# Optimization experiments

Hardware: AMD Instinct MI355X
Metric: run time of the kernel (lower is better)

## Reference

```python
import jax, jax.numpy as jnp
import numpy as np

E = 512
H = 8
D = E // H  # head_dims = 64
MAXREL = 512


def setup_inputs() -> dict:
    key = jax.random.key(0)
    ks = jax.random.split(key, 12)
    B, L = 4, 1024
    s_lin = float(np.sqrt(6.0 / (D + D)))  # xavier uniform for (D,D)
    s_fc = float(np.sqrt(6.0 / (E + E)))
    s_tab = float(np.sqrt(6.0 / (2 * MAXREL + 1 + D)))
    return {
        "query": jax.random.normal(ks[0], (B, L, E), jnp.float32),
        "key": jax.random.normal(ks[1], (B, L, E), jnp.float32),
        "value": jax.random.normal(ks[2], (B, L, E), jnp.float32),
        "mask": jax.random.randint(ks[3], (B, 1, 1, L), 0, 2, jnp.int32),
        "Wq": jax.random.uniform(ks[4], (D, D), jnp.float32, -s_lin, s_lin),
        "bq": jnp.zeros((D,), jnp.float32),
        "Wk": jax.random.uniform(ks[5], (D, D), jnp.float32, -s_lin, s_lin),
        "bk": jnp.zeros((D,), jnp.float32),
        "Wv": jax.random.uniform(ks[6], (D, D), jnp.float32, -s_lin, s_lin),
        "bv": jnp.zeros((D,), jnp.float32),
        "Wfc": jax.random.uniform(ks[7], (E, E), jnp.float32, -s_fc, s_fc),
        "bfc": jnp.zeros((E,), jnp.float32),
        "rel_k_table": jax.random.uniform(ks[8], (2 * MAXREL + 1, D), jnp.float32, -s_tab, s_tab),
        "rel_v_table": jax.random.uniform(ks[9], (2 * MAXREL + 1, D), jnp.float32, -s_tab, s_tab),
    }


def _rel_indices(length_q, length_k):
    dist = jnp.arange(length_k)[None, :] - jnp.arange(length_q)[:, None]
    return jnp.clip(dist, -MAXREL, MAXREL) + MAXREL  # [Q, K]


def reference(query, key, value, mask, Wq, bq, Wk, bk, Wv, bv, Wfc, bfc, rel_k_table, rel_v_table):
    B, Q, _ = query.shape
    K = key.shape[1]
    q = query.reshape(B, Q, H, D) @ Wq.T + bq  # per-head linear (same weights all heads)
    k = key.reshape(B, K, H, D) @ Wk.T + bk
    v = value.reshape(B, K, H, D) @ Wv.T + bv

    scores = jnp.einsum("bqhd,bkhd->bhqk", q, k)  # [B,H,Q,K]
    scores = jnp.where(mask == 0, jnp.float32(-1e20), scores)  # mask BEFORE bias & scale, as in source

    idx = _rel_indices(Q, K)
    a_key = rel_k_table[idx]    # [Q,K,D]
    a_val = rel_v_table[idx]    # [Q,K,D]
    scores = scores + jnp.einsum("bqhd,qkd->bhqk", q, a_key)

    attn = jax.nn.softmax(scores / jnp.sqrt(jnp.float32(D)), axis=-1)

    out = jnp.einsum("bhqk,bkhd->bqhd", attn, v)  # standard AV
    out = out + jnp.einsum("bhqk,qkd->bqhd", attn, a_val)  # relative-position value term
    out = out.reshape(B, Q, H * D)
    return out @ Wfc.T + bfc
```

## Files before the change

### kernel.cpp

```cpp
#include <hip/hip_runtime.h>
#include <math.h>

#define BB 4
#define LL 1024
#define EE 512
#define HH 8
#define DD 64
#define MAXREL 512

typedef unsigned short u16;
typedef __attribute__((ext_vector_type(8))) short bf16x8;
typedef __attribute__((ext_vector_type(4))) float f32x4;

__device__ __forceinline__ u16 f2bf(float f) {
    unsigned int u = __float_as_uint(f);
    unsigned int r = (u + 0x7FFFu + ((u >> 16) & 1u)) >> 16;
    return (u16)r;
}
__device__ __forceinline__ float bf2f(u16 b) {
    return __uint_as_float(((unsigned int)b) << 16);
}
__device__ __forceinline__ bf16x8 ldf8_bf(const float* p) {
    const float4 a = *(const float4*)(p);
    const float4 b = *(const float4*)(p + 4);
    bf16x8 r;
    r[0] = (short)f2bf(a.x); r[1] = (short)f2bf(a.y);
    r[2] = (short)f2bf(a.z); r[3] = (short)f2bf(a.w);
    r[4] = (short)f2bf(b.x); r[5] = (short)f2bf(b.y);
    r[6] = (short)f2bf(b.z); r[7] = (short)f2bf(b.w);
    return r;
}

#define MF(A, B, C) __builtin_amdgcn_mfma_f32_16x16x32_bf16((A), (B), (C), 0, 0, 0)

__global__ __launch_bounds__(256) void proj_mfma_kernel(
    const float* __restrict__ q_in, const float* __restrict__ k_in, const float* __restrict__ v_in,
    const float* __restrict__ Wq, const float* __restrict__ bq,
    const float* __restrict__ Wk, const float* __restrict__ bk,
    const float* __restrict__ Wv, const float* __restrict__ bv,
    u16* __restrict__ qb, u16* __restrict__ kb, u16* __restrict__ vtb)
{
    int bh = blockIdx.x; int b = bh >> 3; int h = bh & 7;
    int l0 = blockIdx.y * 64;
    int t = threadIdx.x; int w = t >> 6; int lane = t & 63;
    int lg = lane >> 4, lc = lane & 15;
    int lt = l0 + w * 16;

    bf16x8 wq[4][2], wk[4][2], wv[4][2];
    #pragma unroll
    for (int dt = 0; dt < 4; ++dt)
        #pragma unroll
        for (int kc = 0; kc < 2; ++kc) {
            int d = dt * 16 + lc, ko = kc * 32 + lg * 8;
            wq[dt][kc] = ldf8_bf(Wq + d * DD + ko);
            wk[dt][kc] = ldf8_bf(Wk + d * DD + ko);
            wv[dt][kc] = ldf8_bf(Wv + d * DD + ko);
        }
    size_t xrow = ((size_t)b * LL + lt + lc) * EE + h * DD;
    bf16x8 xq[2], xk[2], xv[2];
    #pragma unroll
    for (int kc = 0; kc < 2; ++kc) {
        int ko = kc * 32 + lg * 8;
        xq[kc] = ldf8_bf(q_in + xrow + ko);
        xk[kc] = ldf8_bf(k_in + xrow + ko);
        xv[kc] = ldf8_bf(v_in + xrow + ko);
    }

    f32x4 aq[4] = {}, ak[4] = {}, av[4] = {};
    #pragma unroll
    for (int dt = 0; dt < 4; ++dt) {
        aq[dt] = MF(wq[dt][0], xq[0], aq[dt]);
        aq[dt] = MF(wq[dt][1], xq[1], aq[dt]);
        ak[dt] = MF(wk[dt][0], xk[0], ak[dt]);
        ak[dt] = MF(wk[dt][1], xk[1], ak[dt]);
        av[dt] = MF(xv[0], wv[dt][0], av[dt]);
        av[dt] = MF(xv[1], wv[dt][1], av[dt]);
    }

    #pragma unroll
    for (int dt = 0; dt < 4; ++dt) {
        u16 tq[4], tk[4], tv[4];
        #pragma unroll
        for (int r = 0; r < 4; ++r) {
            int d = dt * 16 + lg * 4 + r;
            tq[r] = f2bf(aq[dt][r] + bq[d]);
            tk[r] = f2bf(ak[dt][r] + bk[d]);
            tv[r] = f2bf(av[dt][r] + bv[dt * 16 + lc]);
        }
        size_t o = ((size_t)bh * LL + lt + lc) * DD + dt * 16 + lg * 4;
        *(uint2*)&qb[o] = *(uint2*)tq;
        *(uint2*)&kb[o] = *(uint2*)tk;
        size_t ov = ((size_t)bh * DD + dt * 16 + lc) * LL + lt + lg * 4;
        *(uint2*)&vtb[ov] = *(uint2*)tv;
    }
}

__global__ __launch_bounds__(256) void prep_kernel(
    const float* __restrict__ relk, const float* __restrict__ relv, const float* __restrict__ Wfc,
    u16* __restrict__ relk_pad, u16* __restrict__ relvt_pad, u16* __restrict__ wfcb)
{
    int idx = blockIdx.x * 256 + threadIdx.x;
    if (idx < 2048 * DD) {
        int r = idx >> 6, d = idx & 63;
        int j = r - 512; j = j < 0 ? 0 : (j > 2 * MAXREL ? 2 * MAXREL : j);
        relk_pad[idx] = f2bf(relk[j * DD + d]);
        int dd = idx >> 11, c = idx & 2047;
        int j2 = c - 512; j2 = j2 < 0 ? 0 : (j2 > 2 * MAXREL ? 2 * MAXREL : j2);
        relvt_pad[idx] = f2bf(relv[j2 * DD + dd]);
    }
    if (idx < EE * EE) wfcb[idx] = f2bf(Wfc[idx]);
}

__global__ __launch_bounds__(256) void attn_mfma_kernel(
    const u16* __restrict__ qb, const u16* __restrict__ kb, const u16* __restrict__ vtb,
    const int* __restrict__ mask,
    const u16* __restrict__ relk_pad, const u16* __restrict__ relvt_pad,
    u16* __restrict__ attn_out)
{
    __shared__ __align__(16) char smem[48384];
    u16* Ks   = (u16*)(smem);
    u16* Vts  = (u16*)(smem + 9216);
    u16* RVts = (u16*)(smem + 18432);
    float* lred = (float*)(smem + 48128);
    float* obuf = (float*)smem;

    int bh = blockIdx.x, b = bh >> 3, h = bh & 7;
    int q0 = blockIdx.y * 32;
    int t = threadIdx.x, lane = t & 63, w = t >> 6;
    int rw = w & 1, cw = w >> 1;
    int rbase = rw * 16, c0a = cw * 32;
    int lg = lane >> 4, lc = lane & 15;
    int ub = c0a - rbase + 16;
    size_t bhL = (size_t)bh * LL;
    const u16* kb_bh = kb + bhL * DD;
    const u16* vt_bh = vtb + (size_t)bh * DD * LL;
    const int* mk_b = mask + b * LL;
    u16* Pw  = (u16*)(smem + 33792) + w * 640;
    u16* Pqw = (u16*)(smem + 38912) + w * 1152;

    int su0 = t, su1 = t + 256;
    int sr0 = su0 >> 3, ss0 = (su0 & 7) * 8;
    int sr1 = su1 >> 3, ss1 = (su1 & 7) * 8;
    int rv_row = t >> 2, rv_q = (t & 3) * 24;
    const u16* rvg = relvt_pad + (size_t)rv_row * 2048 + rv_q;
    u16* rvl = RVts + rv_row * 120 + rv_q;
    const u16* rk_base = relk_pad + (size_t)(ub + lc) * DD + lg * 8;

    const u16* qrow = qb + (bhL + q0 + rbase + lc) * DD;
    bf16x8 qf0 = *(const bf16x8*)&qrow[lg * 8];
    bf16x8 qf1 = *(const bf16x8*)&qrow[32 + lg * 8];

    #pragma unroll
    for (int i = 0; i < 3; ++i) {
        int u = lane + i * 64;
        if (u < 144) *(uint4*)&Pqw[u * 8] = make_uint4(0, 0, 0, 0);
    }
    if (t < 192) {
        int row = t / 3, j = t - row * 3;
        *(uint4*)&RVts[row * 120 + 96 + j * 8] = make_uint4(0, 0, 0, 0);
    }
    int sb0 = 992 - q0;
    *(uint4*)&Ks[sr0 * 72 + ss0]  = *(const uint4*)&kb_bh[(size_t)sr0 * DD + ss0];
    *(uint4*)&Ks[sr1 * 72 + ss1]  = *(const uint4*)&kb_bh[(size_t)sr1 * DD + ss1];
    *(uint4*)&Vts[sr0 * 72 + ss0] = *(const uint4*)&vt_bh[(size_t)sr0 * LL + ss0];
    *(uint4*)&Vts[sr1 * 72 + ss1] = *(const uint4*)&vt_bh[(size_t)sr1 * LL + ss1];
    *(uint4*)&rvl[0]  = *(const uint4*)&rvg[sb0];
    *(uint4*)&rvl[8]  = *(const uint4*)&rvg[sb0 + 8];
    *(uint4*)&rvl[16] = *(const uint4*)&rvg[sb0 + 16];
    bf16x8 rk0, rk1, rk2, rk3, rk4, rk5;
    {
        const u16* rkp = rk_base + (size_t)sb0 * DD;
        rk0 = *(const bf16x8*)&rkp[0];
        rk1 = *(const bf16x8*)&rkp[32];
        rk2 = *(const bf16x8*)&rkp[16 * DD];
        rk3 = *(const bf16x8*)&rkp[16 * DD + 32];
        rk4 = *(const bf16x8*)&rkp[32 * DD];
        rk5 = *(const bf16x8*)&rkp[32 * DD + 32];
    }
    __syncthreads();

    f32x4 oacc[4] = {};
    float lacc[4] = {0.f, 0.f, 0.f, 0.f};
    int delta0 = lc - lg * 4;

    #pragma unroll 1
    for (int c = 0; c < 16; ++c) {
        int k0 = c * 64;
        int sb = k0 - q0 + 992;
        int mv0 = mk_b[k0 + c0a + lc];
        int mv1 = mk_b[k0 + c0a + 16 + lc];
        uint4 rK0, rK1, rV0, rV1;
        if (c < 15) {
            int k0n = k0 + 64;
            rK0 = *(const uint4*)&kb_bh[(size_t)(k0n + sr0) * DD + ss0];
            rK1 = *(const uint4*)&kb_bh[(size_t)(k0n + sr1) * DD + ss1];
            rV0 = *(const uint4*)&vt_bh[(size_t)sr0 * LL + k0n + ss0];
            rV1 = *(const uint4*)&vt_bh[(size_t)sr1 * LL + k0n + ss1];
        }

        __builtin_amdgcn_s_setprio(1);
        f32x4 s0 = {}, s1 = {};
        {
            const u16* kp0 = &Ks[(c0a + lc) * 72];
            const u16* kp1 = &Ks[(c0a + 16 + lc) * 72];
            s0 = MF(qf0, *(const bf16x8*)&kp0[lg * 8], s0);
            s0 = MF(qf1, *(const bf16x8*)&kp0[32 + lg * 8], s0);
            s1 = MF(qf0, *(const bf16x8*)&kp1[lg * 8], s1);
            s1 = MF(qf1, *(const bf16x8*)&kp1[32 + lg * 8], s1);
        }
        f32x4 g0 = {}, g1 = {}, g2 = {};
        g0 = MF(qf0, rk0, g0); g0 = MF(qf1, rk1, g0);
        g1 = MF(qf0, rk2, g1); g1 = MF(qf1, rk3, g1);
        g2 = MF(qf0, rk4, g2); g2 = MF(qf1, rk5, g2);
        __builtin_amdgcn_s_setprio(0);

        if (c < 15) {
            const u16* rkp = rk_base + (size_t)(sb + 64) * DD;
            rk0 = *(const bf16x8*)&rkp[0];
            rk1 = *(const bf16x8*)&rkp[32];
            rk2 = *(const bf16x8*)&rkp[16 * DD];
            rk3 = *(const bf16x8*)&rkp[16 * DD + 32];
            rk4 = *(const bf16x8*)&rkp[32 * DD];
            rk5 = *(const bf16x8*)&rkp[32 * DD + 32];
        }

        float mb0 = mv0 ? 0.f : -1e20f;
        float mb1 = mv1 ? 0.f : -1e20f;
        #pragma unroll
        for (int r = 0; r < 4; ++r) {
            int d = delta0 - r;
            int src = (lane & 48) | (d & 15);
            float a0 = __shfl(g0[r], src, 64);
            float a1 = __shfl(g1[r], src, 64);
            float a2 = __shfl(g2[r], src, 64);
            float gv0 = (d >= 0) ? a1 : a0;
            float gv1 = (d >= 0) ? a2 : a1;
            float p0 = __expf((s0[r] + mb0 + gv0) * 0.125f);
            float p1 = __expf((s1[r] + mb1 + gv1) * 0.125f);
            u16 pb0 = f2bf(p0), pb1 = f2bf(p1);
            lacc[r] += bf2f(pb0) + bf2f(pb1);
            int row = lg * 4 + r;
            Pw[row * 40 + lc] = pb0;
            Pw[row * 40 + 16 + lc] = pb1;
            Pqw[row * 72 + lc - row + 16] = pb0;
            Pqw[row * 72 + 32 + lc - row] = pb1;
        }
        asm volatile("s_waitcnt lgkmcnt(0)" ::: "memory");
        __builtin_amdgcn_sched_barrier(0);

        bf16x8 pa  = *(const bf16x8*)&Pw[lc * 40 + lg * 8];
        bf16x8 pq0 = *(const bf16x8*)&Pqw[lc * 72 + lg * 8];
        bf16x8 pq1 = *(const bf16x8*)&Pqw[lc * 72 + 32 + lg * 8];

        __builtin_amdgcn_s_setprio(1);
        #pragma unroll
        for (int dt = 0; dt < 4; ++dt) {
            const u16* vp = &Vts[(dt * 16 + lc) * 72 + c0a];
            const u16* rp = &RVts[(dt * 16 + lc) * 120 + ub];
            oacc[dt] = MF(pa,  *(const bf16x8*)&vp[lg * 8], oacc[dt]);
            oacc[dt] = MF(pq0, *(const bf16x8*)&rp[lg * 8], oacc[dt]);
            oacc[dt] = MF(pq1, *(const bf16x8*)&rp[32 + lg * 8], oacc[dt]);
        }
        __builtin_amdgcn_s_setprio(0);

        if (c < 15) {
            int sbn = sb + 64;
            uint4 b0 = *(const uint4*)&rvg[sbn];
            uint4 b1 = *(const uint4*)&rvg[sbn + 8];
            uint4 b2 = *(const uint4*)&rvg[sbn + 16];
            __syncthreads();
            *(uint4*)&Ks[sr0 * 72 + ss0]  = rK0;
            *(uint4*)&Ks[sr1 * 72 + ss1]  = rK1;
            *(uint4*)&Vts[sr0 * 72 + ss0] = rV0;
            *(uint4*)&Vts[sr1 * 72 + ss1] = rV1;
            *(uint4*)&rvl[0]  = b0;
            *(uint4*)&rvl[8]  = b1;
            *(uint4*)&rvl[16] = b2;
            __syncthreads();
        }
    }

    #pragma unroll
    for (int m2 = 1; m2 <= 8; m2 <<= 1) {
        #pragma unroll
        for (int r = 0; r < 4; ++r) lacc[r] += __shfl_xor(lacc[r], m2);
    }
    if (lc == 0) {
        #pragma unroll
        for (int r = 0; r < 4; ++r) lred[cw * 32 + rbase + lg * 4 + r] = lacc[r];
    }
    __syncthreads();
    if (cw == 1) {
        #pragma unroll
        for (int dt = 0; dt < 4; ++dt)
            #pragma unroll
            for (int r = 0; r < 4; ++r)
                obuf[(rbase + lg * 4 + r) * 68 + dt * 16 + lc] = oacc[dt][r];
    }
    __syncthreads();
    if (cw == 0) {
        float inv[4];
        #pragma unroll
        for (int r = 0; r < 4; ++r) {
            int row = rbase + lg * 4 + r;
            inv[r] = 1.0f / (lred[row] + lred[32 + row]);
        }
        #pragma unroll
        for (int dt = 0; dt < 4; ++dt) {
            #pragma unroll
            for (int r = 0; r < 4; ++r) {
                int row = rbase + lg * 4 + r;
                float v = (oacc[dt][r] + obuf[row * 68 + dt * 16 + lc]) * inv[r];
                attn_out[((size_t)b * LL + q0 + row) * EE + h * DD + dt * 16 + lc] = f2bf(v);
            }
        }
    }
}

__global__ __launch_bounds__(256) void fc_mfma_kernel(
    const u16* __restrict__ Xb, const u16* __restrict__ Wb,
    const float* __restrict__ bfc, float* __restrict__ out)
{
    __shared__ u16 As[128][72];
    __shared__ u16 Bs[128][72];
    int m0 = blockIdx.x * 128, n0 = blockIdx.y * 128;
    int t = threadIdx.x, lane = t & 63, w = t >> 6;
    int rw = w & 1, cw = w >> 1;
    int lg = lane >> 4, lc = lane & 15;
    f32x4 acc[4][4] = {};

    for (int kt = 0; kt < EE; kt += 64) {
        __syncthreads();
        #pragma unroll
        for (int i = 0; i < 4; ++i) {
            int unit = i * 256 + t;
            int row = unit >> 3, s = unit & 7;
            *(uint4*)&As[row][s * 8] = *(const uint4*)&Xb[(size_t)(m0 + row) * EE + kt + s * 8];
            *(uint4*)&Bs[row][s * 8] = *(const uint4*)&Wb[(size_t)(n0 + row) * EE + kt + s * 8];
        }
        __syncthreads();
        #pragma unroll
        for (int kc = 0; kc < 2; ++kc) {
            bf16x8 af[4], bf[4];
            #pragma unroll
            for (int i = 0; i < 4; ++i) {
                af[i] = *(const bf16x8*)&As[rw * 64 + i * 16 + lc][kc * 32 + lg * 8];
                bf[i] = *(const bf16x8*)&Bs[cw * 64 + i * 16 + lc][kc * 32 + lg * 8];
            }
            #pragma unroll
            for (int mi = 0; mi < 4; ++mi)
                #pragma unroll
                for (int ni = 0; ni < 4; ++ni)
                    acc[mi][ni] = MF(af[mi], bf[ni], acc[mi][ni]);
        }
    }
    #pragma unroll
    for (int mi = 0; mi < 4; ++mi) {
        #pragma unroll
        for (int ni = 0; ni < 4; ++ni) {
            int n = n0 + cw * 64 + ni * 16 + lc;
            float bias = bfc[n];
            #pragma unroll
            for (int r = 0; r < 4; ++r) {
                int m = m0 + rw * 64 + mi * 16 + lg * 4 + r;
                out[(size_t)m * EE + n] = acc[mi][ni][r] + bias;
            }
        }
    }
}

extern "C" void kernel_launch(void* const* d_in, const int* in_sizes, int n_in,
                              void* d_out, int out_size, void* d_ws, size_t ws_size,
                              hipStream_t stream) {
    const float* query = (const float*)d_in[0];
    const float* key   = (const float*)d_in[1];
    const float* value = (const float*)d_in[2];
    const int*   mask  = (const int*)d_in[3];
    const float* Wq  = (const float*)d_in[4];
    const float* bq  = (const float*)d_in[5];
    const float* Wk  = (const float*)d_in[6];
    const float* bk  = (const float*)d_in[7];
    const float* Wv  = (const float*)d_in[8];
    const float* bv  = (const float*)d_in[9];
    const float* Wfc = (const float*)d_in[10];
    const float* bfc = (const float*)d_in[11];
    const float* relk = (const float*)d_in[12];
    const float* relv = (const float*)d_in[13];
    float* out = (float*)d_out;

    char* ws = (char*)d_ws;
    u16* qb        = (u16*)(ws);
    u16* kb        = (u16*)(ws + (4u << 20));
    u16* vtb       = (u16*)(ws + (8u << 20));
    u16* attnb     = (u16*)(ws + (12u << 20));
    u16* relk_pad  = (u16*)(ws + (16u << 20));
    u16* relvt_pad = (u16*)(ws + (16u << 20) + 262144);
    u16* wfcb      = (u16*)(ws + (16u << 20) + 524288);

    proj_mfma_kernel<<<dim3(BB * HH, LL / 64), 256, 0, stream>>>(
        query, key, value, Wq, bq, Wk, bk, Wv, bv, qb, kb, vtb);
    prep_kernel<<<1024, 256, 0, stream>>>(relk, relv, Wfc, relk_pad, relvt_pad, wfcb);
    attn_mfma_kernel<<<dim3(BB * HH, LL / 32), 256, 0, stream>>>(
        qb, kb, vtb, mask, relk_pad, relvt_pad, attnb);
    fc_mfma_kernel<<<dim3(BB * LL / 128, EE / 128), 256, 0, stream>>>(attnb, wfcb, bfc, out);
}
```

Baseline: 117.1 us.

## Load K fragments directly to registers, prefetch mask, use exp2 with folded scale

```diff
diff --git a/kernel.cpp b/kernel.cpp
--- a/kernel.cpp
+++ b/kernel.cpp
@@ -32,6 +32,7 @@
 }
 
 #define MF(A, B, C) __builtin_amdgcn_mfma_f32_16x16x32_bf16((A), (B), (C), 0, 0, 0)
+#define EXPSC 0.1803368801111244f
 
 __global__ __launch_bounds__(256) void proj_mfma_kernel(
     const float* __restrict__ q_in, const float* __restrict__ k_in, const float* __restrict__ v_in,
@@ -117,11 +118,10 @@
     const u16* __restrict__ relk_pad, const u16* __restrict__ relvt_pad,
     u16* __restrict__ attn_out)
 {
-    __shared__ __align__(16) char smem[48384];
-    u16* Ks   = (u16*)(smem);
-    u16* Vts  = (u16*)(smem + 9216);
-    u16* RVts = (u16*)(smem + 18432);
-    float* lred = (float*)(smem + 48128);
+    __shared__ __align__(16) char smem[39168];
+    u16* Vts  = (u16*)(smem);
+    u16* RVts = (u16*)(smem + 9216);
+    float* lred = (float*)(smem + 38912);
     float* obuf = (float*)smem;
 
     int bh = blockIdx.x, b = bh >> 3, h = bh & 7;
@@ -135,16 +135,16 @@
     const u16* kb_bh = kb + bhL * DD;
     const u16* vt_bh = vtb + (size_t)bh * DD * LL;
     const int* mk_b = mask + b * LL;
-    u16* Pw  = (u16*)(smem + 33792) + w * 640;
-    u16* Pqw = (u16*)(smem + 38912) + w * 1152;
-
-    int su0 = t, su1 = t + 256;
-    int sr0 = su0 >> 3, ss0 = (su0 & 7) * 8;
-    int sr1 = su1 >> 3, ss1 = (su1 & 7) * 8;
+    u16* Pw  = (u16*)(smem + 24576) + w * 640;
+    u16* Pqw = (u16*)(smem + 29696) + w * 1152;
+
+    int sr0 = t >> 3, ss0 = (t & 7) * 8;
+    int sr1 = sr0 + 32;
     int rv_row = t >> 2, rv_q = (t & 3) * 24;
     const u16* rvg = relvt_pad + (size_t)rv_row * 2048 + rv_q;
     u16* rvl = RVts + rv_row * 120 + rv_q;
     const u16* rk_base = relk_pad + (size_t)(ub + lc) * DD + lg * 8;
+    const u16* kf_base = kb_bh + (size_t)(c0a + lc) * DD + lg * 8;
 
     const u16* qrow = qb + (bhL + q0 + rbase + lc) * DD;
     bf16x8 qf0 = *(const bf16x8*)&qrow[lg * 8];
@@ -160,13 +160,15 @@
         *(uint4*)&RVts[row * 120 + 96 + j * 8] = make_uint4(0, 0, 0, 0);
     }
     int sb0 = 992 - q0;
-    *(uint4*)&Ks[sr0 * 72 + ss0]  = *(const uint4*)&kb_bh[(size_t)sr0 * DD + ss0];
-    *(uint4*)&Ks[sr1 * 72 + ss1]  = *(const uint4*)&kb_bh[(size_t)sr1 * DD + ss1];
     *(uint4*)&Vts[sr0 * 72 + ss0] = *(const uint4*)&vt_bh[(size_t)sr0 * LL + ss0];
-    *(uint4*)&Vts[sr1 * 72 + ss1] = *(const uint4*)&vt_bh[(size_t)sr1 * LL + ss1];
+    *(uint4*)&Vts[sr1 * 72 + ss0] = *(const uint4*)&vt_bh[(size_t)sr1 * LL + ss0];
     *(uint4*)&rvl[0]  = *(const uint4*)&rvg[sb0];
     *(uint4*)&rvl[8]  = *(const uint4*)&rvg[sb0 + 8];
     *(uint4*)&rvl[16] = *(const uint4*)&rvg[sb0 + 16];
+    bf16x8 kf0 = *(const bf16x8*)(kf_base);
+    bf16x8 kf1 = *(const bf16x8*)(kf_base + 32);
+    bf16x8 kf2 = *(const bf16x8*)(kf_base + 16 * DD);
+    bf16x8 kf3 = *(const bf16x8*)(kf_base + 16 * DD + 32);
     bf16x8 rk0, rk1, rk2, rk3, rk4, rk5;
     {
         const u16* rkp = rk_base + (size_t)sb0 * DD;
@@ -177,6 +179,8 @@
         rk4 = *(const bf16x8*)&rkp[32 * DD];
         rk5 = *(const bf16x8*)&rkp[32 * DD + 32];
     }
+    float mb0 = (mk_b[c0a + lc] != 0) ? 0.f : -1e20f;
+    float mb1 = (mk_b[c0a + 16 + lc] != 0) ? 0.f : -1e20f;
     __syncthreads();
 
     f32x4 oacc[4] = {};
@@ -187,27 +191,20 @@
     for (int c = 0; c < 16; ++c) {
         int k0 = c * 64;
         int sb = k0 - q0 + 992;
-        int mv0 = mk_b[k0 + c0a + lc];
-        int mv1 = mk_b[k0 + c0a + 16 + lc];
-        uint4 rK0, rK1, rV0, rV1;
+        uint4 rV0, rV1;
+        float mbn0 = 0.f, mbn1 = 0.f;
         if (c < 15) {
             int k0n = k0 + 64;
-            rK0 = *(const uint4*)&kb_bh[(size_t)(k0n + sr0) * DD + ss0];
-            rK1 = *(const uint4*)&kb_bh[(size_t)(k0n + sr1) * DD + ss1];
             rV0 = *(const uint4*)&vt_bh[(size_t)sr0 * LL + k0n + ss0];
-            rV1 = *(const uint4*)&vt_bh[(size_t)sr1 * LL + k0n + ss1];
+            rV1 = *(const uint4*)&vt_bh[(size_t)sr1 * LL + k0n + ss0];
+            mbn0 = (mk_b[k0n + c0a + lc] != 0) ? 0.f : -1e20f;
+            mbn1 = (mk_b[k0n + c0a + 16 + lc] != 0) ? 0.f : -1e20f;
         }
 
         __builtin_amdgcn_s_setprio(1);
         f32x4 s0 = {}, s1 = {};
-        {
-            const u16* kp0 = &Ks[(c0a + lc) * 72];
-            const u16* kp1 = &Ks[(c0a + 16 + lc) * 72];
-            s0 = MF(qf0, *(const bf16x8*)&kp0[lg * 8], s0);
-            s0 = MF(qf1, *(const bf16x8*)&kp0[32 + lg * 8], s0);
-            s1 = MF(qf0, *(const bf16x8*)&kp1[lg * 8], s1);
-            s1 = MF(qf1, *(const bf16x8*)&kp1[32 + lg * 8], s1);
-        }
+        s0 = MF(qf0, kf0, s0); s0 = MF(qf1, kf1, s0);
+        s1 = MF(qf0, kf2, s1); s1 = MF(qf1, kf3, s1);
         f32x4 g0 = {}, g1 = {}, g2 = {};
         g0 = MF(qf0, rk0, g0); g0 = MF(qf1, rk1, g0);
         g1 = MF(qf0, rk2, g1); g1 = MF(qf1, rk3, g1);
@@ -215,6 +212,11 @@
         __builtin_amdgcn_s_setprio(0);
 
         if (c < 15) {
+            const u16* kfp = kf_base + (size_t)(k0 + 64) * DD;
+            kf0 = *(const bf16x8*)(kfp);
+            kf1 = *(const bf16x8*)(kfp + 32);
+            kf2 = *(const bf16x8*)(kfp + 16 * DD);
+            kf3 = *(const bf16x8*)(kfp + 16 * DD + 32);
             const u16* rkp = rk_base + (size_t)(sb + 64) * DD;
             rk0 = *(const bf16x8*)&rkp[0];
             rk1 = *(const bf16x8*)&rkp[32];
@@ -224,8 +226,6 @@
             rk5 = *(const bf16x8*)&rkp[32 * DD + 32];
         }
 
-        float mb0 = mv0 ? 0.f : -1e20f;
-        float mb1 = mv1 ? 0.f : -1e20f;
         #pragma unroll
         for (int r = 0; r < 4; ++r) {
             int d = delta0 - r;
@@ -235,8 +235,8 @@
             float a2 = __shfl(g2[r], src, 64);
             float gv0 = (d >= 0) ? a1 : a0;
             float gv1 = (d >= 0) ? a2 : a1;
-            float p0 = __expf((s0[r] + mb0 + gv0) * 0.125f);
-            float p1 = __expf((s1[r] + mb1 + gv1) * 0.125f);
+            float p0 = exp2f((s0[r] + mb0 + gv0) * EXPSC);
+            float p1 = exp2f((s1[r] + mb1 + gv1) * EXPSC);
             u16 pb0 = f2bf(p0), pb1 = f2bf(p1);
             lacc[r] += bf2f(pb0) + bf2f(pb1);
             int row = lg * 4 + r;
@@ -245,6 +245,7 @@
             Pqw[row * 72 + lc - row + 16] = pb0;
             Pqw[row * 72 + 32 + lc - row] = pb1;
         }
+        mb0 = mbn0; mb1 = mbn1;
         asm volatile("s_waitcnt lgkmcnt(0)" ::: "memory");
         __builtin_amdgcn_sched_barrier(0);
 
@@ -269,10 +270,8 @@
             uint4 b1 = *(const uint4*)&rvg[sbn + 8];
             uint4 b2 = *(const uint4*)&rvg[sbn + 16];
             __syncthreads();
-            *(uint4*)&Ks[sr0 * 72 + ss0]  = rK0;
-            *(uint4*)&Ks[sr1 * 72 + ss1]  = rK1;
             *(uint4*)&Vts[sr0 * 72 + ss0] = rV0;
-            *(uint4*)&Vts[sr1 * 72 + ss1] = rV1;
+            *(uint4*)&Vts[sr1 * 72 + ss0] = rV1;
             *(uint4*)&rvl[0]  = b0;
             *(uint4*)&rvl[8]  = b1;
             *(uint4*)&rvl[16] = b2;
```

New measurement: 135.8 us. +16.0%, slower.

## Double-buffer relative-key fragments and prefetch mask and rel-V tiles a chunk ahead

Applied to the files above, without the earlier changes.

```diff
diff --git a/kernel.cpp b/kernel.cpp
--- a/kernel.cpp
+++ b/kernel.cpp
@@ -32,6 +32,7 @@
 }
 
 #define MF(A, B, C) __builtin_amdgcn_mfma_f32_16x16x32_bf16((A), (B), (C), 0, 0, 0)
+#define EXPSC 0.1803368801111244f
 
 __global__ __launch_bounds__(256) void proj_mfma_kernel(
     const float* __restrict__ q_in, const float* __restrict__ k_in, const float* __restrict__ v_in,
@@ -138,9 +139,8 @@
     u16* Pw  = (u16*)(smem + 33792) + w * 640;
     u16* Pqw = (u16*)(smem + 38912) + w * 1152;
 
-    int su0 = t, su1 = t + 256;
-    int sr0 = su0 >> 3, ss0 = (su0 & 7) * 8;
-    int sr1 = su1 >> 3, ss1 = (su1 & 7) * 8;
+    int sr0 = t >> 3, ss0 = (t & 7) * 8;
+    int sr1 = sr0 + 32;
     int rv_row = t >> 2, rv_q = (t & 3) * 24;
     const u16* rvg = relvt_pad + (size_t)rv_row * 2048 + rv_q;
     u16* rvl = RVts + rv_row * 120 + rv_q;
@@ -161,124 +161,133 @@
     }
     int sb0 = 992 - q0;
     *(uint4*)&Ks[sr0 * 72 + ss0]  = *(const uint4*)&kb_bh[(size_t)sr0 * DD + ss0];
-    *(uint4*)&Ks[sr1 * 72 + ss1]  = *(const uint4*)&kb_bh[(size_t)sr1 * DD + ss1];
+    *(uint4*)&Ks[sr1 * 72 + ss0]  = *(const uint4*)&kb_bh[(size_t)sr1 * DD + ss0];
     *(uint4*)&Vts[sr0 * 72 + ss0] = *(const uint4*)&vt_bh[(size_t)sr0 * LL + ss0];
-    *(uint4*)&Vts[sr1 * 72 + ss1] = *(const uint4*)&vt_bh[(size_t)sr1 * LL + ss1];
+    *(uint4*)&Vts[sr1 * 72 + ss0] = *(const uint4*)&vt_bh[(size_t)sr1 * LL + ss0];
     *(uint4*)&rvl[0]  = *(const uint4*)&rvg[sb0];
     *(uint4*)&rvl[8]  = *(const uint4*)&rvg[sb0 + 8];
     *(uint4*)&rvl[16] = *(const uint4*)&rvg[sb0 + 16];
-    bf16x8 rk0, rk1, rk2, rk3, rk4, rk5;
+    bf16x8 rkA0, rkA1, rkA2, rkA3, rkA4, rkA5;
+    bf16x8 rkB0, rkB1, rkB2, rkB3, rkB4, rkB5;
     {
         const u16* rkp = rk_base + (size_t)sb0 * DD;
-        rk0 = *(const bf16x8*)&rkp[0];
-        rk1 = *(const bf16x8*)&rkp[32];
-        rk2 = *(const bf16x8*)&rkp[16 * DD];
-        rk3 = *(const bf16x8*)&rkp[16 * DD + 32];
-        rk4 = *(const bf16x8*)&rkp[32 * DD];
-        rk5 = *(const bf16x8*)&rkp[32 * DD + 32];
-    }
+        rkA0 = *(const bf16x8*)&rkp[0];
+        rkA1 = *(const bf16x8*)&rkp[32];
+        rkA2 = *(const bf16x8*)&rkp[16 * DD];
+        rkA3 = *(const bf16x8*)&rkp[16 * DD + 32];
+        rkA4 = *(const bf16x8*)&rkp[32 * DD];
+        rkA5 = *(const bf16x8*)&rkp[32 * DD + 32];
+        const u16* rkq = rk_base + (size_t)(sb0 + 64) * DD;
+        rkB0 = *(const bf16x8*)&rkq[0];
+        rkB1 = *(const bf16x8*)&rkq[32];
+        rkB2 = *(const bf16x8*)&rkq[16 * DD];
+        rkB3 = *(const bf16x8*)&rkq[16 * DD + 32];
+        rkB4 = *(const bf16x8*)&rkq[32 * DD];
+        rkB5 = *(const bf16x8*)&rkq[32 * DD + 32];
+    }
+    float mb0 = (mk_b[c0a + lc] != 0) ? 0.f : -1e20f;
+    float mb1 = (mk_b[c0a + 16 + lc] != 0) ? 0.f : -1e20f;
     __syncthreads();
 
     f32x4 oacc[4] = {};
     float lacc[4] = {0.f, 0.f, 0.f, 0.f};
     int delta0 = lc - lg * 4;
 
+#define CHUNK(C, RK0, RK1, RK2, RK3, RK4, RK5) do { \
+    int k0 = (C) * 64; \
+    int sb_ = k0 - q0 + 992; \
+    uint4 rK0, rK1, rV0, rV1, bb0, bb1, bb2; \
+    float mbn0 = 0.f, mbn1 = 0.f; \
+    if ((C) < 15) { \
+        int k0n = k0 + 64; int sbn_ = sb_ + 64; \
+        rK0 = *(const uint4*)&kb_bh[(size_t)(k0n + sr0) * DD + ss0]; \
+        rK1 = *(const uint4*)&kb_bh[(size_t)(k0n + sr1) * DD + ss0]; \
+        rV0 = *(const uint4*)&vt_bh[(size_t)sr0 * LL + k0n + ss0]; \
+        rV1 = *(const uint4*)&vt_bh[(size_t)sr1 * LL + k0n + ss0]; \
+        bb0 = *(const uint4*)&rvg[sbn_]; \
+        bb1 = *(const uint4*)&rvg[sbn_ + 8]; \
+        bb2 = *(const uint4*)&rvg[sbn_ + 16]; \
+        mbn0 = (mk_b[k0n + c0a + lc] != 0) ? 0.f : -1e20f; \
+        mbn1 = (mk_b[k0n + c0a + 16 + lc] != 0) ? 0.f : -1e20f; \
+    } \
+    __builtin_amdgcn_s_setprio(1); \
+    f32x4 s0 = {}, s1 = {}; \
+    { \
+        const u16* kp0 = &Ks[(c0a + lc) * 72]; \
+        const u16* kp1 = &Ks[(c0a + 16 + lc) * 72]; \
+        s0 = MF(qf0, *(const bf16x8*)&kp0[lg * 8], s0); \
+        s0 = MF(qf1, *(const bf16x8*)&kp0[32 + lg * 8], s0); \
+        s1 = MF(qf0, *(const bf16x8*)&kp1[lg * 8], s1); \
+        s1 = MF(qf1, *(const bf16x8*)&kp1[32 + lg * 8], s1); \
+    } \
+    f32x4 g0 = {}, g1 = {}, g2 = {}; \
+    g0 = MF(qf0, RK0, g0); g0 = MF(qf1, RK1, g0); \
+    g1 = MF(qf0, RK2, g1); g1 = MF(qf1, RK3, g1); \
+    g2 = MF(qf0, RK4, g2); g2 = MF(qf1, RK5, g2); \
+    __builtin_amdgcn_s_setprio(0); \
+    if ((C) < 14) { \
+        const u16* rkp_ = rk_base + (size_t)(sb_ + 128) * DD; \
+        RK0 = *(const bf16x8*)&rkp_[0]; \
+        RK1 = *(const bf16x8*)&rkp_[32]; \
+        RK2 = *(const bf16x8*)&rkp_[16 * DD]; \
+        RK3 = *(const bf16x8*)&rkp_[16 * DD + 32]; \
+        RK4 = *(const bf16x8*)&rkp_[32 * DD]; \
+        RK5 = *(const bf16x8*)&rkp_[32 * DD + 32]; \
+    } \
+    _Pragma("unroll") \
+    for (int r = 0; r < 4; ++r) { \
+        int d_ = delta0 - r; \
+        int src = (lane & 48) | (d_ & 15); \
+        float a0 = __shfl(g0[r], src, 64); \
+        float a1 = __shfl(g1[r], src, 64); \
+        float a2 = __shfl(g2[r], src, 64); \
+        float gv0 = (d_ >= 0) ? a1 : a0; \
+        float gv1 = (d_ >= 0) ? a2 : a1; \
+        float p0 = exp2f((s0[r] + mb0 + gv0) * EXPSC); \
+        float p1 = exp2f((s1[r] + mb1 + gv1) * EXPSC); \
+        u16 pb0 = f2bf(p0), pb1 = f2bf(p1); \
+        lacc[r] += p0 + p1; \
+        int row = lg * 4 + r; \
+        Pw[row * 40 + lc] = pb0; \
+        Pw[row * 40 + 16 + lc] = pb1; \
+        Pqw[row * 72 + lc - row + 16] = pb0; \
+        Pqw[row * 72 + 32 + lc - row] = pb1; \
+    } \
+    mb0 = mbn0; mb1 = mbn1; \
+    asm volatile("s_waitcnt lgkmcnt(0)" ::: "memory"); \
+    __builtin_amdgcn_sched_barrier(0); \
+    bf16x8 pa  = *(const bf16x8*)&Pw[lc * 40 + lg * 8]; \
+    bf16x8 pq0 = *(const bf16x8*)&Pqw[lc * 72 + lg * 8]; \
+    bf16x8 pq1 = *(const bf16x8*)&Pqw[lc * 72 + 32 + lg * 8]; \
+    __builtin_amdgcn_s_setprio(1); \
+    _Pragma("unroll") \
+    for (int dt = 0; dt < 4; ++dt) { \
+        const u16* vp = &Vts[(dt * 16 + lc) * 72 + c0a]; \
+        const u16* rp = &RVts[(dt * 16 + lc) * 120 + ub]; \
+        oacc[dt] = MF(pa,  *(const bf16x8*)&vp[lg * 8], oacc[dt]); \
+        oacc[dt] = MF(pq0, *(const bf16x8*)&rp[lg * 8], oacc[dt]); \
+        oacc[dt] = MF(pq1, *(const bf16x8*)&rp[32 + lg * 8], oacc[dt]); \
+    } \
+    __builtin_amdgcn_s_setprio(0); \
+    if ((C) < 15) { \
+        __syncthreads(); \
+        *(uint4*)&Ks[sr0 * 72 + ss0]  = rK0; \
+        *(uint4*)&Ks[sr1 * 72 + ss0]  = rK1; \
+        *(uint4*)&Vts[sr0 * 72 + ss0] = rV0; \
+        *(uint4*)&Vts[sr1 * 72 + ss0] = rV1; \
+        *(uint4*)&rvl[0]  = bb0; \
+        *(uint4*)&rvl[8]  = bb1; \
+        *(uint4*)&rvl[16] = bb2; \
+        __syncthreads(); \
+    } \
+} while (0)
+
     #pragma unroll 1
-    for (int c = 0; c < 16; ++c) {
-        int k0 = c * 64;
-        int sb = k0 - q0 + 992;
-        int mv0 = mk_b[k0 + c0a + lc];
-        int mv1 = mk_b[k0 + c0a + 16 + lc];
-        uint4 rK0, rK1, rV0, rV1;
-        if (c < 15) {
-            int k0n = k0 + 64;
-            rK0 = *(const uint4*)&kb_bh[(size_t)(k0n + sr0) * DD + ss0];
-            rK1 = *(const uint4*)&kb_bh[(size_t)(k0n + sr1) * DD + ss1];
-            rV0 = *(const uint4*)&vt_bh[(size_t)sr0 * LL + k0n + ss0];
-            rV1 = *(const uint4*)&vt_bh[(size_t)sr1 * LL + k0n + ss1];
-        }
-
-        __builtin_amdgcn_s_setprio(1);
-        f32x4 s0 = {}, s1 = {};
-        {
-            const u16* kp0 = &Ks[(c0a + lc) * 72];
-            const u16* kp1 = &Ks[(c0a + 16 + lc) * 72];
-            s0 = MF(qf0, *(const bf16x8*)&kp0[lg * 8], s0);
-            s0 = MF(qf1, *(const bf16x8*)&kp0[32 + lg * 8], s0);
-            s1 = MF(qf0, *(const bf16x8*)&kp1[lg * 8], s1);
-            s1 = MF(qf1, *(const bf16x8*)&kp1[32 + lg * 8], s1);
-        }
-        f32x4 g0 = {}, g1 = {}, g2 = {};
-        g0 = MF(qf0, rk0, g0); g0 = MF(qf1, rk1, g0);
-        g1 = MF(qf0, rk2, g1); g1 = MF(qf1, rk3, g1);
-        g2 = MF(qf0, rk4, g2); g2 = MF(qf1, rk5, g2);
-        __builtin_amdgcn_s_setprio(0);
-
-        if (c < 15) {
-            const u16* rkp = rk_base + (size_t)(sb + 64) * DD;
-            rk0 = *(const bf16x8*)&rkp[0];
-            rk1 = *(const bf16x8*)&rkp[32];
-            rk2 = *(const bf16x8*)&rkp[16 * DD];
-            rk3 = *(const bf16x8*)&rkp[16 * DD + 32];
-            rk4 = *(const bf16x8*)&rkp[32 * DD];
-            rk5 = *(const bf16x8*)&rkp[32 * DD + 32];
-        }
-
-        float mb0 = mv0 ? 0.f : -1e20f;
-        float mb1 = mv1 ? 0.f : -1e20f;
-        #pragma unroll
-        for (int r = 0; r < 4; ++r) {
-            int d = delta0 - r;
-            int src = (lane & 48) | (d & 15);
-            float a0 = __shfl(g0[r], src, 64);
-            float a1 = __shfl(g1[r], src, 64);
-            float a2 = __shfl(g2[r], src, 64);
-            float gv0 = (d >= 0) ? a1 : a0;
-            float gv1 = (d >= 0) ? a2 : a1;
-            float p0 = __expf((s0[r] + mb0 + gv0) * 0.125f);
-            float p1 = __expf((s1[r] + mb1 + gv1) * 0.125f);
-            u16 pb0 = f2bf(p0), pb1 = f2bf(p1);
-            lacc[r] += bf2f(pb0) + bf2f(pb1);
-            int row = lg * 4 + r;
-            Pw[row * 40 + lc] = pb0;
-            Pw[row * 40 + 16 + lc] = pb1;
-            Pqw[row * 72 + lc - row + 16] = pb0;
-            Pqw[row * 72 + 32 + lc - row] = pb1;
-        }
-        asm volatile("s_waitcnt lgkmcnt(0)" ::: "memory");
-        __builtin_amdgcn_sched_barrier(0);
-
-        bf16x8 pa  = *(const bf16x8*)&Pw[lc * 40 + lg * 8];
-        bf16x8 pq0 = *(const bf16x8*)&Pqw[lc * 72 + lg * 8];
-        bf16x8 pq1 = *(const bf16x8*)&Pqw[lc * 72 + 32 + lg * 8];
-
-        __builtin_amdgcn_s_setprio(1);
-        #pragma unroll
-        for (int dt = 0; dt < 4; ++dt) {
-            const u16* vp = &Vts[(dt * 16 + lc) * 72 + c0a];
-            const u16* rp = &RVts[(dt * 16 + lc) * 120 + ub];
-            oacc[dt] = MF(pa,  *(const bf16x8*)&vp[lg * 8], oacc[dt]);
-            oacc[dt] = MF(pq0, *(const bf16x8*)&rp[lg * 8], oacc[dt]);
-            oacc[dt] = MF(pq1, *(const bf16x8*)&rp[32 + lg * 8], oacc[dt]);
-        }
-        __builtin_amdgcn_s_setprio(0);
-
-        if (c < 15) {
-            int sbn = sb + 64;
-            uint4 b0 = *(const uint4*)&rvg[sbn];
-            uint4 b1 = *(const uint4*)&rvg[sbn + 8];
-            uint4 b2 = *(const uint4*)&rvg[sbn + 16];
-            __syncthreads();
-            *(uint4*)&Ks[sr0 * 72 + ss0]  = rK0;
-            *(uint4*)&Ks[sr1 * 72 + ss1]  = rK1;
-            *(uint4*)&Vts[sr0 * 72 + ss0] = rV0;
-            *(uint4*)&Vts[sr1 * 72 + ss1] = rV1;
-            *(uint4*)&rvl[0]  = b0;
-            *(uint4*)&rvl[8]  = b1;
-            *(uint4*)&rvl[16] = b2;
-            __syncthreads();
-        }
-    }
+    for (int cc = 0; cc < 16; cc += 2) {
+        CHUNK(cc,     rkA0, rkA1, rkA2, rkA3, rkA4, rkA5);
+        CHUNK(cc + 1, rkB0, rkB1, rkB2, rkB3, rkB4, rkB5);
+    }
+#undef CHUNK
 
     #pragma unroll
     for (int m2 = 1; m2 <= 8; m2 <<= 1) {
```

Measured after the change: 153.4 us. 31.1% more time.
